# Kernel tuning notes

Hardware: AMD Instinct MI355X
Metric: run time of the kernel (lower is better)

The kernel has to match this reference:

```python
import jax, jax.numpy as jnp
import numpy as np

B, C, H, W = 32, 512, 28, 28
NUM_CLASSES = 200
THRESHOLD = 0.6


def _conv(x, w, b, pad):
    y = jax.lax.conv_general_dilated(
        x, w, window_strides=(1, 1), padding=[(pad, pad), (pad, pad)],
        dimension_numbers=('NCHW', 'OIHW', 'NCHW'))
    return y + b[None, :, None, None]


def _classifier(x, w1, b1, w2, b2, w3, b3):
    x = jax.nn.relu(_conv(x, w1, b1, 1))
    x = jax.nn.relu(_conv(x, w2, b2, 1))
    return _conv(x, w3, b3, 0)


def _avg_pool3(x):
    # torch F.avg_pool2d(k=3, stride=1, pad=1, count_include_pad=True): sum window / 9
    s = jax.lax.reduce_window(x, 0.0, jax.lax.add, (1, 1, 3, 3), (1, 1, 1, 1),
                              [(0, 0), (0, 0), (1, 1), (1, 1)])
    return s / 9.0


def setup_inputs() -> dict:
    key = jax.random.key(0)
    ks = jax.random.split(key, 16)
    sc = 0.02
    inp = {
        'x': jax.random.normal(ks[0], (B, C, H, W), jnp.float32),
        'label': jax.random.randint(ks[1], (B, NUM_CLASSES), 0, 2),
        'w1a': jax.random.normal(ks[2], (1024, 512, 3, 3), jnp.float32) * sc,
        'b1a': jax.random.normal(ks[3], (1024,), jnp.float32) * sc,
        'w2a': jax.random.normal(ks[4], (1024, 1024, 3, 3), jnp.float32) * sc,
        'b2a': jax.random.normal(ks[5], (1024,), jnp.float32) * sc,
        'w3a': jax.random.normal(ks[6], (NUM_CLASSES, 1024, 1, 1), jnp.float32) * sc,
        'b3a': jax.random.normal(ks[7], (NUM_CLASSES,), jnp.float32) * sc,
        'w1b': jax.random.normal(ks[8], (1024, 512, 3, 3), jnp.float32) * sc,
        'b1b': jax.random.normal(ks[9], (1024,), jnp.float32) * sc,
        'w2b': jax.random.normal(ks[10], (1024, 1024, 3, 3), jnp.float32) * sc,
        'b2b': jax.random.normal(ks[11], (1024,), jnp.float32) * sc,
        'w3b': jax.random.normal(ks[12], (NUM_CLASSES, 1024, 1, 1), jnp.float32) * sc,
        'b3b': jax.random.normal(ks[13], (NUM_CLASSES,), jnp.float32) * sc,
    }
    return inp


def reference(x, label, w1a, b1a, w2a, b2a, w3a, b3a,
              w1b, b1b, w2b, b2b, w3b, b3b):
    feats = _avg_pool3(x)                       # [B,512,H,W]
    out_A = _classifier(feats, w1a, b1a, w2a, b2a, w3a, b3a)  # [B,K,H,W]
    logits_A = out_A.mean(axis=(2, 3))          # [B,K]

    # attention map: per-sample max over channels whose label is nonzero,
    # floored at 0 (the loop seeds the channel stack with a zeros map)
    sel = jnp.where(label[:, :, None, None] > 0, out_A, -jnp.inf)
    atten = jnp.maximum(sel.max(axis=1), 0.0)   # [B,H,W]

    # per-sample min-max normalization over HxW
    mins = atten.min(axis=(1, 2), keepdims=True)
    maxs = atten.max(axis=(1, 2), keepdims=True)
    atten_n = (atten - mins) / (maxs - mins)

    # threshold-erase mask (constant w.r.t. autograd, matching torch code)
    mask = jax.lax.stop_gradient(jnp.where(atten_n >= THRESHOLD, 0.0, 1.0))
    feats_erased = feats * mask[:, None, :, :]

    out_B = _classifier(feats_erased, w1b, b1b, w2b, b2b, w3b, b3b)
    logits_B = out_B.mean(axis=(2, 3))
    return logits_A, logits_B
```

## Files before the change

kernel.cpp:

```cpp
#include <hip/hip_runtime.h>
#include <hip/hip_bf16.h>

typedef unsigned long long ull;
typedef __attribute__((ext_vector_type(8))) short short8;
typedef __attribute__((ext_vector_type(8))) __bf16 bf16x8;
typedef __attribute__((ext_vector_type(4))) float floatx4;

#define GLL16(gp, lp) __builtin_amdgcn_global_load_lds( \
  (__attribute__((address_space(1))) void*)(gp), \
  (__attribute__((address_space(3))) void*)(lp), 16, 0, 0)

#define WVM(N) asm volatile("s_waitcnt vmcnt(" #N ")" ::: "memory")

__device__ __forceinline__ floatx4 mfma16(short8 a, short8 b, floatx4 c){
  return __builtin_amdgcn_mfma_f32_16x16x32_bf16(
      __builtin_bit_cast(bf16x8, a), __builtin_bit_cast(bf16x8, b), c, 0, 0, 0);
}

__device__ __forceinline__ unsigned pkbf(float a, float b){
  unsigned ua = __float_as_uint(a), ub = __float_as_uint(b);
  ua += 0x7fffu + ((ua >> 16) & 1u);
  ub += 0x7fffu + ((ub >> 16) & 1u);
  return (ua >> 16) | (ub & 0xffff0000u);
}

__global__ __launch_bounds__(256) void pool_kernel(const float* __restrict__ x,
                                                   unsigned short* __restrict__ out){
  __shared__ float xs[16*784];
  const int tid = threadIdx.x;
  const int b = blockIdx.x >> 5, cg = blockIdx.x & 31;
  const float* src = x + ((size_t)b*512 + cg*16)*784;
  for (int i=tid;i<16*784;i+=256) xs[i]=src[i];
  __syncthreads();
  unsigned* dst = (unsigned*)out + ((size_t)b*960)*256 + cg*8;
  for (int o=tid;o<30*32*8;o+=256){
    int cip = o & 7, pos = o >> 3;
    int row = pos >> 5, col = pos & 31;
    float s0=0.f, s1=0.f;
    if (row>=1 && row<=28 && col>=1 && col<=28){
      int h=row-1, w=col-1;
      const float* p0 = &xs[(cip*2)*784];
      const float* p1 = p0 + 784;
      #pragma unroll
      for (int dh=-1;dh<=1;++dh){ int hh=h+dh; if ((unsigned)hh<28u){
        #pragma unroll
        for (int dw=-1;dw<=1;++dw){ int ww=w+dw; if((unsigned)ww<28u){
          s0 += p0[hh*28+ww]; s1 += p1[hh*28+ww]; } } } }
      s0 /= 9.f; s1 /= 9.f;
    }
    dst[(size_t)pos*256 + cip] = pkbf(s0, s1);
  }
}

template<int CIN>
__global__ __launch_bounds__(256) void prep3x3(const float* __restrict__ w,
                                               unsigned short* __restrict__ Wt){
  __shared__ float wsm[CIN*9];
  const int co = blockIdx.x, tid = threadIdx.x;
  const float* src = w + (size_t)co*(CIN*9);
  for (int i=tid;i<CIN*9;i+=256) wsm[i]=src[i];
  __syncthreads();
  for (int o=tid;o<9*(CIN/2);o+=256){
    int t = o/(CIN/2), cp = o - t*(CIN/2);
    unsigned v = pkbf(wsm[(cp*2)*9+t], wsm[(cp*2+1)*9+t]);
    ((unsigned*)Wt)[(((size_t)t*1024+co)*CIN>>1) + cp] = v;
  }
}

__global__ __launch_bounds__(256) void prep1x1(const float* __restrict__ w3,
                                               unsigned short* __restrict__ Wp){
  const int row = blockIdx.x, tid = threadIdx.x;
  unsigned* dst = (unsigned*)Wp + (size_t)row*512;
  if (row < 200){
    const float* src = w3 + (size_t)row*1024;
    for (int j=tid;j<512;j+=256) dst[j] = pkbf(src[2*j], src[2*j+1]);
  } else {
    for (int j=tid;j<512;j+=256) dst[j] = 0u;
  }
}

template<int CIN>
__global__ __launch_bounds__(256, 2) void conv3x3_v11(
    const unsigned short* __restrict__ X,
    const unsigned short* __restrict__ Wt,
    const float* __restrict__ bias,
    unsigned short* __restrict__ Out)
{
  constexpr int NCH = CIN/32;
  constexpr size_t CB = (size_t)CIN*2;
  constexpr size_t TAPSTR = (size_t)1024*CB;
  __shared__ char Als[24576];
  __shared__ char Bls[40960];

  const int tid = threadIdx.x;
  const int l = tid & 63, wv = tid >> 6;
  const int cog = wv & 1, pg = wv >> 1;
  const int bid = blockIdx.x;
  const int co0 = (bid & 7) << 7;
  const int y = bid >> 3;
  const int b = y >> 2, rb = y & 3;
  const int r0 = rb << 3;
  const bool active = (pg == 0) || (rb < 3);

  const int sbyt = (l*16) ^ (((l>>3)&7)<<4);
  const int srow = sbyt >> 6;
  const int sw   = sbyt & 63;

  const ull aS0 = (ull)Wt + (size_t)(co0 + (wv*2)*16   + srow)*CB + sw;
  const ull aS1 = (ull)Wt + (size_t)(co0 + (wv*2+1)*16 + srow)*CB + sw;
  ull bS[5];
  #pragma unroll
  for (int k=0;k<5;++k){
    int q = (wv + 4*k)*16 + srow;
    int trow = q >> 5, tcol = q & 31;
    int ir = r0 + trow; if (ir > 29) ir = 29;
    bS[k] = (ull)X + ((size_t)b*960 + ir*32 + tcol)*CB + sw;
  }

  const int jl = l & 15, g = l >> 4;
  int paE[4];
  #pragma unroll
  for (int m=0;m<4;++m){
    int xo = (cog*64 + m*16 + jl)*64 + g*16;
    paE[m] = xo ^ (((xo>>7)&7)<<4);
  }
  int pbS[3][7];
  #pragma unroll
  for (int f=0;f<7;++f){
    int p = pg*112 + f*16 + jl;
    int hl = p/28, cl = p - hl*28;
    #pragma unroll
    for (int ss=0;ss<3;++ss){
      int xo = (hl*32 + cl + ss)*64 + g*16;
      pbS[ss][f] = xo ^ (((xo>>7)&7)<<4);
    }
  }

  floatx4 acc[4][7];
  #pragma unroll
  for (int m=0;m<4;++m)
    #pragma unroll
    for (int f=0;f<7;++f) acc[m][f] = (floatx4){0.f,0.f,0.f,0.f};

  #pragma unroll
  for (int k=0;k<5;++k) GLL16((const void*)bS[k], Bls + (wv + 4*k)*1024);
  GLL16((const void*)aS0,            Als +        (wv*2)*1024);
  GLL16((const void*)aS1,            Als +        (wv*2+1)*1024);
  GLL16((const void*)(aS0 + TAPSTR), Als + 8192 + (wv*2)*1024);
  GLL16((const void*)(aS1 + TAPSTR), Als + 8192 + (wv*2+1)*1024);
  WVM(2);
  __builtin_amdgcn_s_barrier();

  #pragma unroll 1
  for (int c=0;c<NCH;++c){
    const int bbuf = (c&1)*20480;
    #pragma unroll
    for (int t=0;t<9;++t){
      const int rr = t/3, ss = t - rr*3;
      {
        const int stTap = (t<7) ? t+2 : t-7;
        const size_t aoff = (size_t)stTap*TAPSTR + (size_t)(c + (t>=7))*64;
        const int sd = ((t+2)%3)*8192;
        GLL16((const void*)(aS0 + aoff), Als + sd + (wv*2)*1024);
        GLL16((const void*)(aS1 + aoff), Als + sd + (wv*2+1)*1024);
      }
      if (t == 1){
        #pragma unroll
        for (int k=0;k<5;++k)
          GLL16((const void*)(bS[k] + (size_t)(c+1)*64),
                Bls + (bbuf^20480) + (wv + 4*k)*1024);
      }
      short8 a0,a1,a2,a3, bv[7];
      if (active){
        const char* ap = Als + (t%3)*8192;
        a0 = *(const short8*)(ap + paE[0]);
        a1 = *(const short8*)(ap + paE[1]);
        a2 = *(const short8*)(ap + paE[2]);
        a3 = *(const short8*)(ap + paE[3]);
        #pragma unroll
        for (int f=0;f<7;++f)
          bv[f] = *(const short8*)(Bls + bbuf + (pbS[ss][f] + rr*2048));
      }
      __builtin_amdgcn_s_barrier();
      if (active){
        __builtin_amdgcn_s_setprio(1);
        #pragma unroll
        for (int f=0;f<7;++f){
          acc[0][f] = mfma16(a0, bv[f], acc[0][f]);
          acc[1][f] = mfma16(a1, bv[f], acc[1][f]);
          acc[2][f] = mfma16(a2, bv[f], acc[2][f]);
          acc[3][f] = mfma16(a3, bv[f], acc[3][f]);
        }
        __builtin_amdgcn_s_setprio(0);
      }
      if (t == 1) { WVM(7); } else { WVM(2); }
      __builtin_amdgcn_s_barrier();
    }
  }

  if (!active) return;

  #pragma unroll
  for (int m=0;m<4;++m){
    const int coL = cog*64 + m*16 + g*4;
    const float4 bv4 = *(const float4*)&bias[co0 + coL];
    #pragma unroll
    for (int f=0;f<7;++f){
      int pp = pg*112 + f*16 + jl;
      int hl = pp/28, cl = pp - hl*28;
      float v0 = fmaxf(acc[m][f][0] + bv4.x, 0.f);
      float v1 = fmaxf(acc[m][f][1] + bv4.y, 0.f);
      float v2 = fmaxf(acc[m][f][2] + bv4.z, 0.f);
      float v3 = fmaxf(acc[m][f][3] + bv4.w, 0.f);
      uint2 pk; pk.x = pkbf(v0,v1); pk.y = pkbf(v2,v3);
      size_t oa = ((size_t)b*960 + (size_t)(r0 + hl + 1)*32 + (cl + 1))*1024 + (co0 + coL);
      *(uint2*)(Out + oa) = pk;
    }
  }
}

template<int CIN, bool K3, bool BF16OUT>
__global__ __launch_bounds__(512, 2) void conv_mfma(
    const unsigned short* __restrict__ X,
    const unsigned short* __restrict__ Wt,
    const float* __restrict__ bias, int biasN,
    void* __restrict__ Out)
{
  constexpr int T9 = K3 ? 9 : 1;
  constexpr int NA = K3 ? 9 : 1;
  __shared__ short Als[T9*4096];
  __shared__ short Bls[10240];
  __shared__ float biasLs[128];

  const int tid = threadIdx.x;
  const int l = tid & 63, wv = tid >> 6;
  const int wc = wv & 3, wp = wv >> 2;
  const int co0 = blockIdx.x << 7;
  const int by = blockIdx.y;
  const int b = by >> 2, rb = by & 3;
  const int r0 = rb << 3;
  const int nrh = (rb < 3) ? 10 : 6;
  const int NB = 2*nrh;
  const bool active = (wp == 0) || (rb < 3);

  if (tid < 128) biasLs[tid] = (co0 + tid < biasN) ? bias[co0 + tid] : 0.f;

  const size_t laneOff = (size_t)(l >> 2)*(CIN*2) + (size_t)(l & 3)*16;

  ull aB[NA];
  #pragma unroll
  for (int j=0;j<NA;++j){
    int k = wv*NA + j;
    int t = K3 ? (k >> 3) : 0;
    int cog2 = K3 ? (k & 7) : k;
    aB[j] = (ull)Wt + ((size_t)(t*1024 + co0 + cog2*16)*(CIN*2)) + laneOff;
  }
  const ull xBase = (ull)X + ((size_t)b*960)*(CIN*2) + (size_t)(r0*32)*(CIN*2) + laneOff;
  ull bB0=0, bB1=0, bB2=0; int nb=0;
  if (wv < NB)      { bB0 = xBase + (size_t)(wv*16)*(CIN*2);      nb = 1; }
  if (wv + 8 < NB)  { bB1 = xBase + (size_t)((wv+8)*16)*(CIN*2);  nb = 2; }
  if (wv + 16 < NB) { bB2 = xBase + (size_t)((wv+16)*16)*(CIN*2); nb = 3; }

  const int jl = l & 15, g = l >> 4;
  int paE[2];
  #pragma unroll
  for (int m=0;m<2;++m) paE[m] = (wc*32 + m*16 + jl)*32 + g*8;
  int pbE[7], ph[7], pc[7];
  #pragma unroll
  for (int f=0;f<7;++f){
    int p = wp*112 + f*16 + jl;
    int hl = p / 28, cl = p - hl*28;
    ph[f]=hl; pc[f]=cl;
    pbE[f] = (hl*32 + cl)*32 + g*8;
  }

  floatx4 acc[2][7];
  #pragma unroll
  for (int m=0;m<2;++m)
    #pragma unroll
    for (int f=0;f<7;++f) acc[m][f] = (floatx4){0.f,0.f,0.f,0.f};

  const int NCH = CIN/32;
  for (int c=0;c<NCH;++c){
    if (c) __syncthreads();
    const size_t cOff = (size_t)c*64;
    #pragma unroll
    for (int j=0;j<NA;++j)
      GLL16((const void*)(aB[j] + cOff), (char*)Als + (wv*NA + j)*1024);
    GLL16((const void*)(bB0 + cOff), (char*)Bls + wv*1024);
    if (nb > 1) GLL16((const void*)(bB1 + cOff), (char*)Bls + (wv+8)*1024);
    if (nb > 2) GLL16((const void*)(bB2 + cOff), (char*)Bls + (wv+16)*1024);
    __syncthreads();
    if (active){
      #pragma unroll
      for (int t=0;t<T9;++t){
        const int tA = t*4096;
        const int tB = K3 ? (((t/3)*32 + (t - (t/3)*3))*32) : ((1*32+1)*32);
        short8 a0 = *(const short8*)&Als[tA + paE[0]];
        short8 a1 = *(const short8*)&Als[tA + paE[1]];
        #pragma unroll
        for (int f=0;f<7;++f){
          short8 bvv = *(const short8*)&Bls[tB + pbE[f]];
          acc[0][f] = mfma16(a0, bvv, acc[0][f]);
          acc[1][f] = mfma16(a1, bvv, acc[1][f]);
        }
      }
    }
  }

  if (!active) return;

  #pragma unroll
  for (int m=0;m<2;++m){
    const int coL = wc*32 + m*16 + g*4;
    const float4 bv4 = *(const float4*)&biasLs[coL];
    #pragma unroll
    for (int f=0;f<7;++f){
      float v0 = acc[m][f][0] + bv4.x;
      float v1 = acc[m][f][1] + bv4.y;
      float v2 = acc[m][f][2] + bv4.z;
      float v3 = acc[m][f][3] + bv4.w;
      if constexpr (BF16OUT){
        v0=fmaxf(v0,0.f); v1=fmaxf(v1,0.f); v2=fmaxf(v2,0.f); v3=fmaxf(v3,0.f);
        uint2 pk; pk.x = pkbf(v0,v1); pk.y = pkbf(v2,v3);
        size_t oa = ((size_t)b*960 + (size_t)(r0 + ph[f] + 1)*32 + (pc[f]+1))*1024 + (co0 + coL);
        *(uint2*)((unsigned short*)Out + oa) = pk;
      } else {
        int co = co0 + coL;
        if (co < 200){
          int p = wp*112 + f*16 + jl;
          size_t oa = ((size_t)b*784 + (size_t)(r0*28) + p)*200 + co;
          float4 ov; ov.x=v0; ov.y=v1; ov.z=v2; ov.w=v3;
          *(float4*)((float*)Out + oa) = ov;
        }
      }
    }
  }
}

__global__ __launch_bounds__(256) void logits_kernel(const float* __restrict__ outC,
                                                     float* __restrict__ dst){
  const int b = blockIdx.x, seg = blockIdx.y;
  const int co = threadIdx.x;
  if (co >= 200) return;
  const float* base = outC + ((size_t)b*784 + seg*98)*200 + co;
  float s = 0.f;
  for (int p=0;p<98;++p) s += base[(size_t)p*200];
  atomicAdd(&dst[b*200+co], s*(1.f/784.f));
}

__global__ __launch_bounds__(256) void atten_kernel(const float* __restrict__ outC,
                                                    const int* __restrict__ label,
                                                    float* __restrict__ mask){
  __shared__ float al[784];
  __shared__ float redn[256], redx[256];
  __shared__ unsigned char lab[200];
  const int b = blockIdx.x, tid = threadIdx.x;
  for (int i=tid;i<200;i+=256) lab[i] = label[b*200+i] > 0 ? 1 : 0;
  __syncthreads();
  for (int p=tid;p<784;p+=256){
    const float* row = outC + ((size_t)b*784+p)*200;
    float m = -__builtin_inff();
    for (int c=0;c<200;++c) if (lab[c]) m = fmaxf(m, row[c]);
    al[p] = fmaxf(m, 0.f);
  }
  __syncthreads();
  float mn = __builtin_inff(), mx = -__builtin_inff();
  for (int p=tid;p<784;p+=256){ float v=al[p]; mn=fminf(mn,v); mx=fmaxf(mx,v); }
  redn[tid]=mn; redx[tid]=mx; __syncthreads();
  for (int s2=128;s2>0;s2>>=1){
    if (tid<s2){ redn[tid]=fminf(redn[tid],redn[tid+s2]); redx[tid]=fmaxf(redx[tid],redx[tid+s2]); }
    __syncthreads();
  }
  mn = redn[0]; mx = redx[0];
  for (int p=tid;p<784;p+=256){
    float nrm = (al[p]-mn)/(mx-mn);
    mask[b*784+p] = (nrm >= 0.6f) ? 0.f : 1.f;
  }
}

__global__ __launch_bounds__(256) void erase_kernel(const unsigned short* __restrict__ feats,
                                                    const float* __restrict__ mask,
                                                    unsigned short* __restrict__ dst){
  const int blk = blockIdx.x; const int b = blk/30, row = blk - b*30;
  const size_t base = ((size_t)b*960 + row*32)*512;
  for (int i=threadIdx.x; i<4096; i+=256){
    int col = i >> 7;
    float mv = 0.f;
    if (row>=1 && row<=28 && col>=1 && col<=28) mv = mask[b*784 + (row-1)*28 + (col-1)];
    uint2 v = make_uint2(0u,0u);
    if (mv > 0.5f) v = *(const uint2*)(feats + base + (size_t)i*4);
    *(uint2*)(dst + base + (size_t)i*4) = v;
  }
}

extern "C" void kernel_launch(void* const* d_in, const int* in_sizes, int n_in,
                              void* d_out, int out_size, void* d_ws, size_t ws_size,
                              hipStream_t stream){
  (void)in_sizes; (void)n_in; (void)out_size; (void)ws_size;
  const float* x   = (const float*)d_in[0];
  const int* label = (const int*)d_in[1];
  const float* w1a = (const float*)d_in[2];  const float* b1a = (const float*)d_in[3];
  const float* w2a = (const float*)d_in[4];  const float* b2a = (const float*)d_in[5];
  const float* w3a = (const float*)d_in[6];  const float* b3a = (const float*)d_in[7];
  const float* w1b = (const float*)d_in[8];  const float* b1b = (const float*)d_in[9];
  const float* w2b = (const float*)d_in[10]; const float* b2b = (const float*)d_in[11];
  const float* w3b = (const float*)d_in[12]; const float* b3b = (const float*)d_in[13];

  char* ws = (char*)d_ws;
  unsigned short* WtS = (unsigned short*)(ws);
  unsigned short* WtL = (unsigned short*)(ws + 9441280);
  unsigned short* W3p = (unsigned short*)(ws + 28319744);
  unsigned short* F   = (unsigned short*)(ws + 28848128);
  unsigned short* G1  = (unsigned short*)(ws + 60309504);
  unsigned short* G2  = (unsigned short*)(ws + 123228160);
  float* outC  = (float*)(ws + 186146816);
  float* maskB = (float*)(ws + 206217216);
  float* logA = (float*)d_out;
  float* logB = logA + 6400;

  hipMemsetAsync(G1, 0, 62914560, stream);
  hipMemsetAsync(G2, 0, 62914560, stream);
  hipMemsetAsync(d_out, 0, 51200, stream);

  pool_kernel<<<1024,256,0,stream>>>(x, F);

  prep3x3<512><<<1024,256,0,stream>>>(w1a, WtS);
  conv3x3_v11<512><<<1024,256,0,stream>>>(F, WtS, b1a, G1);
  prep3x3<1024><<<1024,256,0,stream>>>(w2a, WtL);
  conv3x3_v11<1024><<<1024,256,0,stream>>>(G1, WtL, b2a, G2);
  prep1x1<<<256,256,0,stream>>>(w3a, W3p);
  conv_mfma<1024,false,false><<<dim3(2,128),512,0,stream>>>(G2, W3p, b3a, 200, outC);
  logits_kernel<<<dim3(32,8),256,0,stream>>>(outC, logA);
  atten_kernel<<<32,256,0,stream>>>(outC, label, maskB);
  erase_kernel<<<960,256,0,stream>>>(F, maskB, G1);

  prep3x3<512><<<1024,256,0,stream>>>(w1b, WtS);
  conv3x3_v11<512><<<1024,256,0,stream>>>(G1, WtS, b1b, G2);
  prep3x3<1024><<<1024,256,0,stream>>>(w2b, WtL);
  conv3x3_v11<1024><<<1024,256,0,stream>>>(G2, WtL, b2b, G1);
  prep1x1<<<256,256,0,stream>>>(w3b, W3p);
  conv_mfma<1024,false,false><<<dim3(2,128),512,0,stream>>>(G1, W3p, b3b, 200, outC);
  logits_kernel<<<dim3(32,8),256,0,stream>>>(outC, logB);
}
```

Baseline: 1.500 ms.

## Double-buffer LDS fragments in registers and drop one barrier per tap

The 3x3 conv main loop now preloads the A and B fragments for the next tap into a second register set while the MFMAs for the current tap run. This removes the barrier that sat between the LDS reads and the MFMAs, leaving one barrier per tap. The channel loop is unrolled by two so the buffer indices resolve at compile time. The cost is higher VGPR pressure under launch_bounds(256,2), with a risk of spills or lower occupancy, plus one extra speculative LDS prefetch at the end of the loop.

```diff
diff --git a/kernel.cpp b/kernel.cpp
--- a/kernel.cpp
+++ b/kernel.cpp
@@ -80,7 +80,7 @@
 }
 
 template<int CIN>
-__global__ __launch_bounds__(256, 2) void conv3x3_v11(
+__global__ __launch_bounds__(256, 2) void conv3x3_v12(
     const unsigned short* __restrict__ X,
     const unsigned short* __restrict__ Wt,
     const float* __restrict__ bias,
@@ -142,6 +142,8 @@
     #pragma unroll
     for (int f=0;f<7;++f) acc[m][f] = (floatx4){0.f,0.f,0.f,0.f};
 
+  short8 fa[2][4], fb[2][7];
+
   #pragma unroll
   for (int k=0;k<5;++k) GLL16((const void*)bS[k], Bls + (wv + 4*k)*1024);
   GLL16((const void*)aS0,            Als +        (wv*2)*1024);
@@ -150,50 +152,55 @@
   GLL16((const void*)(aS1 + TAPSTR), Als + 8192 + (wv*2+1)*1024);
   WVM(2);
   __builtin_amdgcn_s_barrier();
+  if (active){
+    #pragma unroll
+    for (int m=0;m<4;++m) fa[0][m] = *(const short8*)(Als + paE[m]);
+    #pragma unroll
+    for (int f=0;f<7;++f) fb[0][f] = *(const short8*)(Bls + pbS[0][f]);
+  }
 
   #pragma unroll 1
-  for (int c=0;c<NCH;++c){
-    const int bbuf = (c&1)*20480;
-    #pragma unroll
-    for (int t=0;t<9;++t){
-      const int rr = t/3, ss = t - rr*3;
+  for (int c=0;c<NCH;c+=2){
+    #pragma unroll
+    for (int tt=0;tt<18;++tt){
+      const int t  = tt % 9;
+      const int ch = c + tt/9;
       {
         const int stTap = (t<7) ? t+2 : t-7;
-        const size_t aoff = (size_t)stTap*TAPSTR + (size_t)(c + (t>=7))*64;
-        const int sd = ((t+2)%3)*8192;
+        const size_t aoff = (size_t)stTap*TAPSTR + (size_t)(ch + (t>=7))*64;
+        const int sd = ((tt+2)%3)*8192;
         GLL16((const void*)(aS0 + aoff), Als + sd + (wv*2)*1024);
         GLL16((const void*)(aS1 + aoff), Als + sd + (wv*2+1)*1024);
       }
       if (t == 1){
         #pragma unroll
         for (int k=0;k<5;++k)
-          GLL16((const void*)(bS[k] + (size_t)(c+1)*64),
-                Bls + (bbuf^20480) + (wv + 4*k)*1024);
-      }
-      short8 a0,a1,a2,a3, bv[7];
+          GLL16((const void*)(bS[k] + (size_t)(ch+1)*64),
+                Bls + (((ch+1)&1)*20480) + (wv + 4*k)*1024);
+      }
+      if (t == 1) { WVM(7); } else { WVM(2); }
       if (active){
-        const char* ap = Als + (t%3)*8192;
-        a0 = *(const short8*)(ap + paE[0]);
-        a1 = *(const short8*)(ap + paE[1]);
-        a2 = *(const short8*)(ap + paE[2]);
-        a3 = *(const short8*)(ap + paE[3]);
+        const int tn  = (t+1) % 9;
+        const int rrn = tn/3, ssn = tn - rrn*3;
+        const char* ap = Als + ((tt+1)%3)*8192;
+        const int bb = (((tt+1)/9)&1)*20480;
+        #pragma unroll
+        for (int m=0;m<4;++m) fa[(tt+1)&1][m] = *(const short8*)(ap + paE[m]);
         #pragma unroll
         for (int f=0;f<7;++f)
-          bv[f] = *(const short8*)(Bls + bbuf + (pbS[ss][f] + rr*2048));
-      }
-      __builtin_amdgcn_s_barrier();
+          fb[(tt+1)&1][f] = *(const short8*)(Bls + bb + pbS[ssn][f] + rrn*2048);
+      }
       if (active){
         __builtin_amdgcn_s_setprio(1);
         #pragma unroll
         for (int f=0;f<7;++f){
-          acc[0][f] = mfma16(a0, bv[f], acc[0][f]);
-          acc[1][f] = mfma16(a1, bv[f], acc[1][f]);
-          acc[2][f] = mfma16(a2, bv[f], acc[2][f]);
-          acc[3][f] = mfma16(a3, bv[f], acc[3][f]);
+          acc[0][f] = mfma16(fa[tt&1][0], fb[tt&1][f], acc[0][f]);
+          acc[1][f] = mfma16(fa[tt&1][1], fb[tt&1][f], acc[1][f]);
+          acc[2][f] = mfma16(fa[tt&1][2], fb[tt&1][f], acc[2][f]);
+          acc[3][f] = mfma16(fa[tt&1][3], fb[tt&1][f], acc[3][f]);
         }
         __builtin_amdgcn_s_setprio(0);
       }
-      if (t == 1) { WVM(7); } else { WVM(2); }
       __builtin_amdgcn_s_barrier();
     }
   }
@@ -426,9 +433,9 @@
   pool_kernel<<<1024,256,0,stream>>>(x, F);
 
   prep3x3<512><<<1024,256,0,stream>>>(w1a, WtS);
-  conv3x3_v11<512><<<1024,256,0,stream>>>(F, WtS, b1a, G1);
+  conv3x3_v12<512><<<1024,256,0,stream>>>(F, WtS, b1a, G1);
   prep3x3<1024><<<1024,256,0,stream>>>(w2a, WtL);
-  conv3x3_v11<1024><<<1024,256,0,stream>>>(G1, WtL, b2a, G2);
+  conv3x3_v12<1024><<<1024,256,0,stream>>>(G1, WtL, b2a, G2);
   prep1x1<<<256,256,0,stream>>>(w3a, W3p);
   conv_mfma<1024,false,false><<<dim3(2,128),512,0,stream>>>(G2, W3p, b3a, 200, outC);
   logits_kernel<<<dim3(32,8),256,0,stream>>>(outC, logA);
@@ -436,9 +443,9 @@
   erase_kernel<<<960,256,0,stream>>>(F, maskB, G1);
 
   prep3x3<512><<<1024,256,0,stream>>>(w1b, WtS);
-  conv3x3_v11<512><<<1024,256,0,stream>>>(G1, WtS, b1b, G2);
+  conv3x3_v12<512><<<1024,256,0,stream>>>(G1, WtS, b1b, G2);
   prep3x3<1024><<<1024,256,0,stream>>>(w2b, WtL);
-  conv3x3_v11<1024><<<1024,256,0,stream>>>(G2, WtL, b2b, G1);
+  conv3x3_v12<1024><<<1024,256,0,stream>>>(G2, WtL, b2b, G1);
   prep1x1<<<256,256,0,stream>>>(w3b, W3p);
   conv_mfma<1024,false,false><<<dim3(2,128),512,0,stream>>>(G1, W3p, b3b, 200, outC);
   logits_kernel<<<dim3(32,8),256,0,stream>>>(outC, logB);
```

Result: slower. 1.682 ms (+12.1%).
